# Kernel tuning notes

Hardware: AMD Instinct MI355X
Metric: run time of the kernel (lower is better)

## Reference

```python
import jax, jax.numpy as jnp
import numpy as np

N_GENES = 20000
UNITS = 10000
DEG = 32
BATCH = 128

def setup_inputs() -> dict:
    key = jax.random.key(0)
    k1, k2, k3, k4 = jax.random.split(key, 4)
    feature = jax.random.normal(k1, (BATCH, N_GENES), dtype=jnp.float32)
    ppi = jax.random.randint(k2, (UNITS, DEG), 0, N_GENES, dtype=jnp.int64)
    kernel = jax.random.normal(k3, (UNITS,), dtype=jnp.float32)
    bias = jax.random.normal(k4, (UNITS,), dtype=jnp.float32)
    return {"feature": feature, "ppi": ppi, "kernel": kernel, "bias": bias}

def reference(feature, ppi, kernel, bias):
    # gather along gene axis: [B, UNITS, DEG]
    h = jnp.abs(feature[:, ppi])
    # sum over neighbors -> [B, UNITS]
    h = jnp.sum(h, axis=-1)
    h = h * kernel + bias
    return jnp.tanh(h)
```

## Files before the change

### kernel.cpp

```cpp
#include <hip/hip_runtime.h>
#include <hip/hip_fp16.h>
#include <math.h>

#define N_GENES 20000
#define UNITS   10000
#define DEG     32
#define BATCH   128

__global__ __launch_bounds__(256) void transpose_abs_f16_kernel(
    const float* __restrict__ in, __half* __restrict__ out)
{
    __shared__ float tile[32][33];
    const int g0 = blockIdx.x * 32;
    const int b0 = blockIdx.y * 32;
    const int tx = threadIdx.x;
    const int ty = threadIdx.y;
#pragma unroll
    for (int i = 0; i < 32; i += 8)
        tile[ty + i][tx] = fabsf(in[(size_t)(b0 + ty + i) * N_GENES + (g0 + tx)]);
    __syncthreads();
#pragma unroll
    for (int i = 0; i < 32; i += 8)
        out[(size_t)(g0 + ty + i) * BATCH + (b0 + tx)] = __float2half(tile[tx][ty + i]);
}

__global__ __launch_bounds__(256) void gather_unit_kernel(
    const __half2* __restrict__ featT,
    const int*   __restrict__ ppi,
    const float* __restrict__ kernelw,
    const float* __restrict__ bias,
    float*       __restrict__ out)
{
    __shared__ int idx[8 * DEG];
    const int tid = threadIdx.x;
    const int u0  = blockIdx.x * 8;

    idx[tid] = ppi[(size_t)u0 * DEG + tid];
    __syncthreads();

    const int lane = tid & 63;
    const int w    = tid >> 6;
    const int ub   = w * 2;

    float2 acc0 = {0.f, 0.f}, acc1 = {0.f, 0.f};

#pragma unroll 8
    for (int d = 0; d < DEG; ++d) {
        const int g0 = idx[ub * DEG + d];
        const int g1 = idx[(ub + 1) * DEG + d];
        const float2 f0 = __half22float2(featT[(size_t)g0 * 64 + lane]);
        const float2 f1 = __half22float2(featT[(size_t)g1 * 64 + lane]);
        acc0.x += f0.x; acc0.y += f0.y;
        acc1.x += f1.x; acc1.y += f1.y;
    }

    const int u  = u0 + ub;
    const float k0 = kernelw[u],     k1 = kernelw[u + 1];
    const float c0 = bias[u],        c1 = bias[u + 1];

    const float h00 = acc0.x * k0 + c0;
    const float h01 = acc1.x * k1 + c1;
    const float h10 = acc0.y * k0 + c0;
    const float h11 = acc1.y * k1 + c1;
    const float r00 = 1.f - 2.f / (__expf(2.f * h00) + 1.f);
    const float r01 = 1.f - 2.f / (__expf(2.f * h01) + 1.f);
    const float r10 = 1.f - 2.f / (__expf(2.f * h10) + 1.f);
    const float r11 = 1.f - 2.f / (__expf(2.f * h11) + 1.f);

    const int b = lane * 2;
    *(float2*)(out + (size_t)b       * UNITS + u) = make_float2(r00, r01);
    *(float2*)(out + (size_t)(b + 1) * UNITS + u) = make_float2(r10, r11);
}

extern "C" void kernel_launch(void* const* d_in, const int* in_sizes, int n_in,
                              void* d_out, int out_size, void* d_ws, size_t ws_size,
                              hipStream_t stream) {
    const float* feature = (const float*)d_in[0];
    const int*   ppi     = (const int*)d_in[1];
    const float* kernelw = (const float*)d_in[2];
    const float* bias    = (const float*)d_in[3];
    float* out   = (float*)d_out;
    __half* featT = (__half*)d_ws;

    dim3 g1(N_GENES / 32, BATCH / 32);
    dim3 b1(32, 8);
    transpose_abs_f16_kernel<<<g1, b1, 0, stream>>>(feature, featT);

    gather_unit_kernel<<<UNITS / 8, 256, 0, stream>>>(
        (const __half2*)featT, ppi, kernelw, bias, out);
}
```

Baseline: 79.96 us.

## Split transposed features into batch planes and gather each plane separately

Lays out the abs-transposed fp16 features as two 64-column batch planes and launches the gather kernel once per plane. Each wave splits its lanes across neighbour parity and reduces with a cross-half shuffle, and the outputs use nontemporal stores. The aim is a smaller working set per launch for better cache hit rates during the random gather. It adds a second launch, re-reads the indices and leaves half the lanes idle in the epilogue.

```diff
diff --git a/kernel.cpp b/kernel.cpp
--- a/kernel.cpp
+++ b/kernel.cpp
@@ -6,6 +6,7 @@
 #define UNITS   10000
 #define DEG     32
 #define BATCH   128
+#define UPB     8
 
 __global__ __launch_bounds__(256) void transpose_abs_f16_kernel(
     const float* __restrict__ in, __half* __restrict__ out)
@@ -19,57 +20,71 @@
     for (int i = 0; i < 32; i += 8)
         tile[ty + i][tx] = fabsf(in[(size_t)(b0 + ty + i) * N_GENES + (g0 + tx)]);
     __syncthreads();
+    const int b  = b0 + tx;
+    const size_t plane = (size_t)(b >> 6) * N_GENES * 64;
+    const int bp = b & 63;
 #pragma unroll
     for (int i = 0; i < 32; i += 8)
-        out[(size_t)(g0 + ty + i) * BATCH + (b0 + tx)] = __float2half(tile[tx][ty + i]);
+        out[plane + (size_t)(g0 + ty + i) * 64 + bp] = __float2half(tile[tx][ty + i]);
 }
 
-__global__ __launch_bounds__(256) void gather_unit_kernel(
-    const __half2* __restrict__ featT,
+__global__ __launch_bounds__(256) void gather_half_kernel(
+    const __half2* __restrict__ plane,
     const int*   __restrict__ ppi,
     const float* __restrict__ kernelw,
     const float* __restrict__ bias,
-    float*       __restrict__ out)
+    float*       __restrict__ outh)
 {
-    __shared__ int idx[8 * DEG];
+    __shared__ int idx[UPB * DEG];
     const int tid = threadIdx.x;
-    const int u0  = blockIdx.x * 8;
+    const int u0  = blockIdx.x * UPB;
 
     idx[tid] = ppi[(size_t)u0 * DEG + tid];
     __syncthreads();
 
     const int lane = tid & 63;
     const int w    = tid >> 6;
+    const int dh   = lane >> 5;
+    const int c    = lane & 31;
     const int ub   = w * 2;
 
     float2 acc0 = {0.f, 0.f}, acc1 = {0.f, 0.f};
-
-#pragma unroll 8
-    for (int d = 0; d < DEG; ++d) {
+#pragma unroll
+    for (int it = 0; it < 16; ++it) {
+        const int d  = it * 2 + dh;
         const int g0 = idx[ub * DEG + d];
         const int g1 = idx[(ub + 1) * DEG + d];
-        const float2 f0 = __half22float2(featT[(size_t)g0 * 64 + lane]);
-        const float2 f1 = __half22float2(featT[(size_t)g1 * 64 + lane]);
+        const float2 f0 = __half22float2(plane[(size_t)g0 * 32 + c]);
+        const float2 f1 = __half22float2(plane[(size_t)g1 * 32 + c]);
         acc0.x += f0.x; acc0.y += f0.y;
         acc1.x += f1.x; acc1.y += f1.y;
     }
+    acc0.x += __shfl_xor(acc0.x, 32, 64);
+    acc0.y += __shfl_xor(acc0.y, 32, 64);
+    acc1.x += __shfl_xor(acc1.x, 32, 64);
+    acc1.y += __shfl_xor(acc1.y, 32, 64);
 
-    const int u  = u0 + ub;
-    const float k0 = kernelw[u],     k1 = kernelw[u + 1];
-    const float c0 = bias[u],        c1 = bias[u + 1];
+    if (dh == 0) {
+        const int u  = u0 + ub;
+        const float k0 = kernelw[u],     k1 = kernelw[u + 1];
+        const float c0 = bias[u],        c1 = bias[u + 1];
+        const float h00 = acc0.x * k0 + c0;
+        const float h10 = acc1.x * k1 + c1;
+        const float h01 = acc0.y * k0 + c0;
+        const float h11 = acc1.y * k1 + c1;
+        const float r00 = 1.f - 2.f / (__expf(2.f * h00) + 1.f);
+        const float r10 = 1.f - 2.f / (__expf(2.f * h10) + 1.f);
+        const float r01 = 1.f - 2.f / (__expf(2.f * h01) + 1.f);
+        const float r11 = 1.f - 2.f / (__expf(2.f * h11) + 1.f);
 
-    const float h00 = acc0.x * k0 + c0;
-    const float h01 = acc1.x * k1 + c1;
-    const float h10 = acc0.y * k0 + c0;
-    const float h11 = acc1.y * k1 + c1;
-    const float r00 = 1.f - 2.f / (__expf(2.f * h00) + 1.f);
-    const float r01 = 1.f - 2.f / (__expf(2.f * h01) + 1.f);
-    const float r10 = 1.f - 2.f / (__expf(2.f * h10) + 1.f);
-    const float r11 = 1.f - 2.f / (__expf(2.f * h11) + 1.f);
-
-    const int b = lane * 2;
-    *(float2*)(out + (size_t)b       * UNITS + u) = make_float2(r00, r01);
-    *(float2*)(out + (size_t)(b + 1) * UNITS + u) = make_float2(r10, r11);
+        const int b = c * 2;
+        float2 v0 = make_float2(r00, r10);
+        float2 v1 = make_float2(r01, r11);
+        __builtin_nontemporal_store(*(const double*)&v0,
+            (double*)(outh + (size_t)b * UNITS + u));
+        __builtin_nontemporal_store(*(const double*)&v1,
+            (double*)(outh + (size_t)(b + 1) * UNITS + u));
+    }
 }
 
 extern "C" void kernel_launch(void* const* d_in, const int* in_sizes, int n_in,
@@ -79,13 +94,17 @@
     const int*   ppi     = (const int*)d_in[1];
     const float* kernelw = (const float*)d_in[2];
     const float* bias    = (const float*)d_in[3];
-    float* out   = (float*)d_out;
+    float* out = (float*)d_out;
     __half* featT = (__half*)d_ws;
 
     dim3 g1(N_GENES / 32, BATCH / 32);
     dim3 b1(32, 8);
     transpose_abs_f16_kernel<<<g1, b1, 0, stream>>>(feature, featT);
 
-    gather_unit_kernel<<<UNITS / 8, 256, 0, stream>>>(
-        (const __half2*)featT, ppi, kernelw, bias, out);
+    const __half2* plane0 = (const __half2*)featT;
+    const __half2* plane1 = (const __half2*)(featT + (size_t)N_GENES * 64);
+    gather_half_kernel<<<UNITS / UPB, 256, 0, stream>>>(
+        plane0, ppi, kernelw, bias, out);
+    gather_half_kernel<<<UNITS / UPB, 256, 0, stream>>>(
+        plane1, ppi, kernelw, bias, out + (size_t)64 * UNITS);
 }
```

Result: slower. 88.93 us (+11.2%).
